# Kernel optimization log

Hardware: AMD Instinct MI355X
Metric: run time of the kernel (lower is better)

The kernel has to match this reference:

```python
import jax, jax.numpy as jnp
import numpy as np
import math

Z, H, G, S = 4, 16, 4, 4096          # batch, q heads, kv groups, seq len
BLOCK = 32                            # compression block size
NB = S // BLOCK                       # number of compressed KV blocks (128)
DQK, DV = 128, 128                    # head dims


def setup_inputs() -> dict:
    key = jax.random.key(0)
    k1, k2, k3 = jax.random.split(key, 3)
    q = jax.random.normal(k1, (Z, H, S, DQK), jnp.float32)
    k_blocks = jax.random.normal(k2, (Z, G, NB, DQK), jnp.float32)
    v_blocks = jax.random.normal(k3, (Z, G, NB, DV), jnp.float32)
    # block j covers tokens [j*BLOCK, (j+1)*BLOCK), so it 'ends' at position (j+1)*BLOCK-1
    block_ends = (jnp.arange(1, NB + 1) * BLOCK - 1).astype(jnp.int32)
    return {"q": q, "k_blocks": k_blocks, "v_blocks": v_blocks, "block_ends": block_ends}


def reference(q, k_blocks, v_blocks, block_ends):
    """NSA compression attention fwd: block-end causal masking over compressed KV blocks.
    q: [Z,H,S,Dqk]; k_blocks/v_blocks: [Z,G,NB,D]; block_ends: [NB] int.
    Query at position m attends to compressed block j iff block_ends[j] <= m.
    Rows with no valid block output zeros (matching the kernel's l_i==0 path)."""
    Zb, Hb, Sb, Dq = q.shape
    Gb = k_blocks.shape[1]
    sm_scale = 1.0 / math.sqrt(Dq)
    # GQA: head h -> kv group h // (H // G)
    qg = (q * sm_scale).reshape(Zb, Gb, Hb // Gb, Sb, Dq)
    s = jnp.einsum('zghsd,zgnd->zghsn', qg, k_blocks)        # [Z,G,H/G,S,NB]
    pos = jnp.arange(Sb)
    mask = block_ends[None, :] <= pos[:, None]               # [S,NB]
    s_masked = jnp.where(mask, s, -jnp.inf)
    m = jnp.max(s_masked, axis=-1, keepdims=True)            # online-softmax max (M)
    m_safe = jnp.where(jnp.isfinite(m), m, 0.0)
    p = jnp.where(mask, jnp.exp(s_masked - jax.lax.stop_gradient(m_safe)), 0.0)
    l = jnp.sum(p, axis=-1, keepdims=True)                   # softmax denom (exp(L-M))
    o = jnp.einsum('zghsn,zgnv->zghsv', p, v_blocks)
    o = jnp.where(l > 0, o / jnp.where(l > 0, l, 1.0), 0.0)
    return o.reshape(Zb, Hb, Sb, -1)                         # [Z,H,S,Dv]
```

## Files before the change

### kernel.cpp

```cpp
#include <hip/hip_runtime.h>


#define Zc 4
#define Hc 16
#define Gc 4
#define Sc 4096
#define NBc 128
#define Dc 128
#define VST 136

typedef __attribute__((ext_vector_type(8))) short short8;
typedef __attribute__((ext_vector_type(4))) float float4v;

__device__ inline unsigned pk2bf(float a, float b) {
    union { float f; unsigned u; } x, y; x.f = a; y.f = b;
    return __builtin_amdgcn_perm(y.u + 0x8000u, x.u + 0x8000u, 0x07060302u);
}
__device__ inline short8 mkfrag(float4v f0, float4v f1) {
    union { short8 v; unsigned d[4]; } u;
    u.d[0] = pk2bf(f0[0], f0[1]);
    u.d[1] = pk2bf(f0[2], f0[3]);
    u.d[2] = pk2bf(f1[0], f1[1]);
    u.d[3] = pk2bf(f1[2], f1[3]);
    return u.v;
}

__global__ __launch_bounds__(256, 4)
void nsa_fwd(const float* __restrict__ q, const float* __restrict__ kb,
             const float* __restrict__ vb, float* __restrict__ out) {
    __shared__ __align__(16) short KV[NBc * VST];

    const int bx   = blockIdx.x, m0 = bx * 128;
    const int h    = blockIdx.y, z = blockIdx.z, g = h >> 2;
    const int tid  = threadIdx.x;
    const int wq   = tid >> 6;
    const int lane = tid & 63;
    const int l16  = lane & 15;
    const int quad = lane >> 4;

    const int nvmax   = 4 * bx + 4;
    const int c_max   = (nvmax + 15) >> 4;
    const int kbi_max = (nvmax + 31) >> 5;
    const int nstage  = kbi_max << 5;

    const float* qbase = q + ((size_t)(z * Hc + h) * Sc + m0 + wq * 32) * Dc;
    float4v qraw[4][2][2];
    #pragma unroll
    for (int dk = 0; dk < 4; dk++)
        #pragma unroll
        for (int t = 0; t < 2; t++) {
            const float* s = qbase + (size_t)(t * 16 + l16) * Dc + dk * 32 + quad * 8;
            qraw[dk][t][0] = *(const float4v*)s;
            qraw[dk][t][1] = *(const float4v*)(s + 4);
        }

    const float* ksrc = kb + (size_t)(z * Gc + g) * NBc * Dc;
    #pragma unroll
    for (int it = 0; it < 8; it++)
        if (it < c_max) {
            int i = it * 256 + tid;
            int n = i >> 4, c8 = i & 15;
            const float* s = ksrc + (size_t)n * Dc + c8 * 8;
            float4v f0 = *(const float4v*)s, f1 = *(const float4v*)(s + 4);
            *(short8*)(KV + n * VST + c8 * 8) = mkfrag(f0, f1);
        }

    const float sm = 0.08838834764831845f;
    short8 qf[4][2];
    #pragma unroll
    for (int dk = 0; dk < 4; dk++)
        #pragma unroll
        for (int t = 0; t < 2; t++)
            qf[dk][t] = mkfrag(qraw[dk][t][0] * sm, qraw[dk][t][1] * sm);

    __syncthreads();

    float4v acc[8][2];
    #pragma unroll
    for (int c = 0; c < 8; c++)
        #pragma unroll
        for (int t = 0; t < 2; t++) acc[c][t] = (float4v)0.f;

    #pragma unroll
    for (int dk = 0; dk < 4; dk++)
        #pragma unroll
        for (int c = 0; c < 8; c++)
            if (c < c_max) {
                short8 a = *(const short8*)(KV + (c * 16 + l16) * VST + dk * 32 + quad * 8);
                acc[c][0] = __builtin_amdgcn_mfma_f32_16x16x32_bf16(a, qf[dk][0], acc[c][0], 0, 0, 0);
                acc[c][1] = __builtin_amdgcn_mfma_f32_16x16x32_bf16(a, qf[dk][1], acc[c][1], 0, 0, 0);
            }

    __syncthreads();

    {
        const float* vsrc = vb + (size_t)(z * Gc + g) * NBc * Dc;
        const int np = tid & 63, n2 = np * 2;
        const bool vact = (n2 < nstage);
        #pragma unroll
        for (int it = 0; it < 8; it++) {
            const int c = it * 4 + wq;
            if (vact) {
                float4v fa = *(const float4v*)(vsrc + (size_t)n2 * Dc + c * 4);
                float4v fb = *(const float4v*)(vsrc + (size_t)(n2 + 1) * Dc + c * 4);
                #pragma unroll
                for (int k2 = 0; k2 < 4; k2++)
                    *(unsigned*)(KV + (c * 4 + k2) * VST + n2) = pk2bf(fa[k2], fb[k2]);
            }
        }
    }

    unsigned Ppk[8][2][2];
    #pragma unroll
    for (int c = 0; c < 8; c++)
        #pragma unroll
        for (int t = 0; t < 2; t++) { Ppk[c][t][0] = 0u; Ppk[c][t][1] = 0u; }

    #pragma unroll
    for (int t = 0; t < 2; t++) {
        const int mg = m0 + wq * 32 + t * 16 + l16;
        int nv = (mg + 1) >> 5; if (nv > NBc) nv = NBc;
        float mx = -1e30f;
        #pragma unroll
        for (int c = 0; c < 8; c++)
            if (c < c_max)
                #pragma unroll
                for (int r = 0; r < 4; r++) {
                    const int j = c * 16 + quad * 4 + r;
                    float s = acc[c][t][r];
                    s = (j < nv) ? s : -1e30f;
                    acc[c][t][r] = s;
                    mx = fmaxf(mx, s);
                }
        mx = fmaxf(mx, __shfl_xor(mx, 16, 64));
        mx = fmaxf(mx, __shfl_xor(mx, 32, 64));
        float ls = 0.f;
        #pragma unroll
        for (int c = 0; c < 8; c++)
            if (c < c_max)
                #pragma unroll
                for (int r = 0; r < 4; r++) {
                    float s = acc[c][t][r];
                    float p = (s > -1e29f) ? __expf(s - mx) : 0.f;
                    acc[c][t][r] = p;
                    ls += p;
                }
        ls += __shfl_xor(ls, 16, 64);
        ls += __shfl_xor(ls, 32, 64);
        const float inv = (ls > 0.f) ? 1.f / ls : 0.f;
        #pragma unroll
        for (int c = 0; c < 8; c++)
            if (c < c_max) {
                Ppk[c][t][0] = pk2bf(acc[c][t][0] * inv, acc[c][t][1] * inv);
                Ppk[c][t][1] = pk2bf(acc[c][t][2] * inv, acc[c][t][3] * inv);
            }
    }

    __syncthreads();

    float4v oacc[8][2];
    #pragma unroll
    for (int c = 0; c < 8; c++)
        #pragma unroll
        for (int t = 0; t < 2; t++) oacc[c][t] = (float4v)0.f;

    const int s0 = (((2 * quad) & 3) << 4) | l16;
    const int s1 = (((2 * quad + 1) & 3) << 4) | l16;
    const bool hi = (quad >= 2);

    #pragma unroll
    for (int kbi = 0; kbi < 4; kbi++)
        if (kbi < kbi_max) {
            short8 ap[2];
            #pragma unroll
            for (int t = 0; t < 2; t++) {
                const int c1 = 2 * kbi;
                unsigned w0a = (unsigned)__shfl((int)Ppk[c1    ][t][0], s0, 64);
                unsigned w0b = (unsigned)__shfl((int)Ppk[c1 + 1][t][0], s0, 64);
                unsigned w1a = (unsigned)__shfl((int)Ppk[c1    ][t][1], s0, 64);
                unsigned w1b = (unsigned)__shfl((int)Ppk[c1 + 1][t][1], s0, 64);
                unsigned w2a = (unsigned)__shfl((int)Ppk[c1    ][t][0], s1, 64);
                unsigned w2b = (unsigned)__shfl((int)Ppk[c1 + 1][t][0], s1, 64);
                unsigned w3a = (unsigned)__shfl((int)Ppk[c1    ][t][1], s1, 64);
                unsigned w3b = (unsigned)__shfl((int)Ppk[c1 + 1][t][1], s1, 64);
                union { short8 v; unsigned d[4]; } u;
                u.d[0] = hi ? w0b : w0a;
                u.d[1] = hi ? w1b : w1a;
                u.d[2] = hi ? w2b : w2a;
                u.d[3] = hi ? w3b : w3a;
                ap[t] = u.v;
            }
            #pragma unroll
            for (int c = 0; c < 8; c++) {
                short8 bv = *(const short8*)(KV + (c * 16 + l16) * VST + kbi * 32 + quad * 8);
                #pragma unroll
                for (int t = 0; t < 2; t++)
                    oacc[c][t] = __builtin_amdgcn_mfma_f32_16x16x32_bf16(ap[t], bv, oacc[c][t], 0, 0, 0);
            }
        }

    float* obase = out + ((size_t)(z * Hc + h) * Sc + m0 + wq * 32) * Dc;
    #pragma unroll
    for (int t = 0; t < 2; t++)
        #pragma unroll
        for (int rr = 0; rr < 4; rr++) {
            const int row = t * 16 + quad * 4 + rr;
            #pragma unroll
            for (int c = 0; c < 8; c++)
                obase[(size_t)row * Dc + c * 16 + l16] = oacc[c][t][rr];
        }
}

extern "C" void kernel_launch(void* const* d_in, const int* in_sizes, int n_in,
                              void* d_out, int out_size, void* d_ws, size_t ws_size,
                              hipStream_t stream) {
    const float* q  = (const float*)d_in[0];
    const float* kb = (const float*)d_in[1];
    const float* vb = (const float*)d_in[2];
    float* out = (float*)d_out;
    dim3 grid(Sc / 128, Hc, Zc);
    nsa_fwd<<<grid, dim3(256), 0, stream>>>(q, kb, vb, out);
}
```

Before: 257.4 us.

## Pair causal query tiles per block to balance work and share KV staging

Each block now handles two 128-row query tiles, b and 31-b, so every block does roughly the same amount of causal work. The K and V blocks are staged to LDS once for both tiles. Per-warp limits (cmax/kbi) now bound the MFMA loops at warp rather than block granularity. The V global loads are issued into registers ahead of the second QK GEMM to overlap latency, which raises register pressure; the launch bound drops to 2 blocks per CU and the grid halves to 1024 blocks.

```diff
diff --git a/kernel.cpp b/kernel.cpp
--- a/kernel.cpp
+++ b/kernel.cpp
@@ -25,100 +25,32 @@
     return u.v;
 }
 
-__global__ __launch_bounds__(256, 4)
-void nsa_fwd(const float* __restrict__ q, const float* __restrict__ kb,
-             const float* __restrict__ vb, float* __restrict__ out) {
-    __shared__ __align__(16) short KV[NBc * VST];
-
-    const int bx   = blockIdx.x, m0 = bx * 128;
-    const int h    = blockIdx.y, z = blockIdx.z, g = h >> 2;
-    const int tid  = threadIdx.x;
-    const int wq   = tid >> 6;
-    const int lane = tid & 63;
-    const int l16  = lane & 15;
-    const int quad = lane >> 4;
-
-    const int nvmax   = 4 * bx + 4;
-    const int c_max   = (nvmax + 15) >> 4;
-    const int kbi_max = (nvmax + 31) >> 5;
-    const int nstage  = kbi_max << 5;
-
-    const float* qbase = q + ((size_t)(z * Hc + h) * Sc + m0 + wq * 32) * Dc;
-    float4v qraw[4][2][2];
-    #pragma unroll
-    for (int dk = 0; dk < 4; dk++)
-        #pragma unroll
-        for (int t = 0; t < 2; t++) {
-            const float* s = qbase + (size_t)(t * 16 + l16) * Dc + dk * 32 + quad * 8;
-            qraw[dk][t][0] = *(const float4v*)s;
-            qraw[dk][t][1] = *(const float4v*)(s + 4);
-        }
-
-    const float* ksrc = kb + (size_t)(z * Gc + g) * NBc * Dc;
-    #pragma unroll
-    for (int it = 0; it < 8; it++)
-        if (it < c_max) {
-            int i = it * 256 + tid;
-            int n = i >> 4, c8 = i & 15;
-            const float* s = ksrc + (size_t)n * Dc + c8 * 8;
-            float4v f0 = *(const float4v*)s, f1 = *(const float4v*)(s + 4);
-            *(short8*)(KV + n * VST + c8 * 8) = mkfrag(f0, f1);
-        }
-
-    const float sm = 0.08838834764831845f;
-    short8 qf[4][2];
-    #pragma unroll
-    for (int dk = 0; dk < 4; dk++)
-        #pragma unroll
-        for (int t = 0; t < 2; t++)
-            qf[dk][t] = mkfrag(qraw[dk][t][0] * sm, qraw[dk][t][1] * sm);
-
-    __syncthreads();
-
-    float4v acc[8][2];
+__device__ inline void do_gemm1(const short* __restrict__ Ksh, short8 (&qf)[4][2],
+                                float4v (&acc)[8][2], int c_max, int l16, int quad) {
     #pragma unroll
     for (int c = 0; c < 8; c++)
         #pragma unroll
         for (int t = 0; t < 2; t++) acc[c][t] = (float4v)0.f;
-
     #pragma unroll
     for (int dk = 0; dk < 4; dk++)
         #pragma unroll
         for (int c = 0; c < 8; c++)
             if (c < c_max) {
-                short8 a = *(const short8*)(KV + (c * 16 + l16) * VST + dk * 32 + quad * 8);
+                short8 a = *(const short8*)(Ksh + (c * 16 + l16) * VST + dk * 32 + quad * 8);
                 acc[c][0] = __builtin_amdgcn_mfma_f32_16x16x32_bf16(a, qf[dk][0], acc[c][0], 0, 0, 0);
                 acc[c][1] = __builtin_amdgcn_mfma_f32_16x16x32_bf16(a, qf[dk][1], acc[c][1], 0, 0, 0);
             }
-
-    __syncthreads();
-
-    {
-        const float* vsrc = vb + (size_t)(z * Gc + g) * NBc * Dc;
-        const int np = tid & 63, n2 = np * 2;
-        const bool vact = (n2 < nstage);
-        #pragma unroll
-        for (int it = 0; it < 8; it++) {
-            const int c = it * 4 + wq;
-            if (vact) {
-                float4v fa = *(const float4v*)(vsrc + (size_t)n2 * Dc + c * 4);
-                float4v fb = *(const float4v*)(vsrc + (size_t)(n2 + 1) * Dc + c * 4);
-                #pragma unroll
-                for (int k2 = 0; k2 < 4; k2++)
-                    *(unsigned*)(KV + (c * 4 + k2) * VST + n2) = pk2bf(fa[k2], fb[k2]);
-            }
-        }
-    }
-
-    unsigned Ppk[8][2][2];
+}
+
+__device__ inline void do_softmax(float4v (&acc)[8][2], unsigned (&Ppk)[8][2][2],
+                                  int m0, int c_max, int l16, int quad) {
     #pragma unroll
     for (int c = 0; c < 8; c++)
         #pragma unroll
         for (int t = 0; t < 2; t++) { Ppk[c][t][0] = 0u; Ppk[c][t][1] = 0u; }
-
     #pragma unroll
     for (int t = 0; t < 2; t++) {
-        const int mg = m0 + wq * 32 + t * 16 + l16;
+        const int mg = m0 + t * 16 + l16;
         int nv = (mg + 1) >> 5; if (nv > NBc) nv = NBc;
         float mx = -1e30f;
         #pragma unroll
@@ -155,9 +87,11 @@
                 Ppk[c][t][1] = pk2bf(acc[c][t][2] * inv, acc[c][t][3] * inv);
             }
     }
-
-    __syncthreads();
-
+}
+
+__device__ inline void do_gemm2_store(const short* __restrict__ Vt, unsigned (&Ppk)[8][2][2],
+                                      float* __restrict__ obase, int kbi_max,
+                                      int l16, int quad) {
     float4v oacc[8][2];
     #pragma unroll
     for (int c = 0; c < 8; c++)
@@ -192,14 +126,13 @@
             }
             #pragma unroll
             for (int c = 0; c < 8; c++) {
-                short8 bv = *(const short8*)(KV + (c * 16 + l16) * VST + kbi * 32 + quad * 8);
+                short8 bv = *(const short8*)(Vt + (c * 16 + l16) * VST + kbi * 32 + quad * 8);
                 #pragma unroll
                 for (int t = 0; t < 2; t++)
                     oacc[c][t] = __builtin_amdgcn_mfma_f32_16x16x32_bf16(ap[t], bv, oacc[c][t], 0, 0, 0);
             }
         }
 
-    float* obase = out + ((size_t)(z * Hc + h) * Sc + m0 + wq * 32) * Dc;
     #pragma unroll
     for (int t = 0; t < 2; t++)
         #pragma unroll
@@ -209,6 +142,122 @@
             for (int c = 0; c < 8; c++)
                 obase[(size_t)row * Dc + c * 16 + l16] = oacc[c][t][rr];
         }
+}
+
+__global__ __launch_bounds__(256, 2)
+void nsa_fwd(const float* __restrict__ q, const float* __restrict__ kb,
+             const float* __restrict__ vb, float* __restrict__ out) {
+    __shared__ __align__(16) short KV[NBc * VST];
+
+    const int b    = blockIdx.x;
+    const int h    = blockIdx.y, z = blockIdx.z, g = h >> 2;
+    const int tid  = threadIdx.x;
+    const int wq   = tid >> 6;
+    const int lane = tid & 63;
+    const int l16  = lane & 15;
+    const int quad = lane >> 4;
+
+    const int bx0 = b, bx1 = 31 - b;
+    const int nv0 = 4 * bx0 + wq + 1;
+    const int nv1 = 4 * bx1 + wq + 1;
+    const int cmax0 = (nv0 + 15) >> 4, kbi0 = (nv0 + 31) >> 5;
+    const int cmax1 = (nv1 + 15) >> 4, kbi1 = (nv1 + 31) >> 5;
+    const int nv_hi  = 4 * bx1 + 4;
+    const int cst    = (nv_hi + 15) >> 4;
+    const int nstage = ((nv_hi + 31) >> 5) << 5;
+
+    const int m0_0 = bx0 * 128 + wq * 32;
+    const int m0_1 = bx1 * 128 + wq * 32;
+    const float sm = 0.08838834764831845f;
+
+    const float* qb0 = q + ((size_t)(z * Hc + h) * Sc + m0_0) * Dc;
+    float4v q0raw[4][2][2];
+    #pragma unroll
+    for (int dk = 0; dk < 4; dk++)
+        #pragma unroll
+        for (int t = 0; t < 2; t++) {
+            const float* s = qb0 + (size_t)(t * 16 + l16) * Dc + dk * 32 + quad * 8;
+            q0raw[dk][t][0] = *(const float4v*)s;
+            q0raw[dk][t][1] = *(const float4v*)(s + 4);
+        }
+
+    const float* ksrc = kb + (size_t)(z * Gc + g) * NBc * Dc;
+    #pragma unroll
+    for (int it = 0; it < 8; it++)
+        if (it < cst) {
+            int i = it * 256 + tid;
+            int n = i >> 4, c8 = i & 15;
+            const float* s = ksrc + (size_t)n * Dc + c8 * 8;
+            float4v f0 = *(const float4v*)s, f1 = *(const float4v*)(s + 4);
+            *(short8*)(KV + n * VST + c8 * 8) = mkfrag(f0, f1);
+        }
+
+    short8 qf[4][2];
+    #pragma unroll
+    for (int dk = 0; dk < 4; dk++)
+        #pragma unroll
+        for (int t = 0; t < 2; t++)
+            qf[dk][t] = mkfrag(q0raw[dk][t][0] * sm, q0raw[dk][t][1] * sm);
+
+    __syncthreads();
+
+    const float* qb1 = q + ((size_t)(z * Hc + h) * Sc + m0_1) * Dc;
+    float4v q1raw[4][2][2];
+    #pragma unroll
+    for (int dk = 0; dk < 4; dk++)
+        #pragma unroll
+        for (int t = 0; t < 2; t++) {
+            const float* s = qb1 + (size_t)(t * 16 + l16) * Dc + dk * 32 + quad * 8;
+            q1raw[dk][t][0] = *(const float4v*)s;
+            q1raw[dk][t][1] = *(const float4v*)(s + 4);
+        }
+
+    float4v acc[8][2];
+    unsigned Ppk0[8][2][2], Ppk1[8][2][2];
+
+    do_gemm1(KV, qf, acc, cmax0, l16, quad);
+    do_softmax(acc, Ppk0, m0_0, cmax0, l16, quad);
+
+    #pragma unroll
+    for (int dk = 0; dk < 4; dk++)
+        #pragma unroll
+        for (int t = 0; t < 2; t++)
+            qf[dk][t] = mkfrag(q1raw[dk][t][0] * sm, q1raw[dk][t][1] * sm);
+
+    const float* vsrc = vb + (size_t)(z * Gc + g) * NBc * Dc;
+    const int n2 = lane * 2;
+    const bool vact = (n2 < nstage);
+    float4v vraw[8][2];
+    #pragma unroll
+    for (int it = 0; it < 8; it++) {
+        const int c = it * 4 + wq;
+        if (vact) {
+            vraw[it][0] = *(const float4v*)(vsrc + (size_t)n2 * Dc + c * 4);
+            vraw[it][1] = *(const float4v*)(vsrc + (size_t)(n2 + 1) * Dc + c * 4);
+        }
+    }
+
+    do_gemm1(KV, qf, acc, cmax1, l16, quad);
+
+    __syncthreads();
+
+    #pragma unroll
+    for (int it = 0; it < 8; it++) {
+        const int c = it * 4 + wq;
+        if (vact) {
+            #pragma unroll
+            for (int k2 = 0; k2 < 4; k2++)
+                *(unsigned*)(KV + (c * 4 + k2) * VST + n2) = pk2bf(vraw[it][0][k2], vraw[it][1][k2]);
+        }
+    }
+    do_softmax(acc, Ppk1, m0_1, cmax1, l16, quad);
+
+    __syncthreads();
+
+    float* ob0 = out + ((size_t)(z * Hc + h) * Sc + m0_0) * Dc;
+    float* ob1 = out + ((size_t)(z * Hc + h) * Sc + m0_1) * Dc;
+    do_gemm2_store(KV, Ppk0, ob0, kbi0, l16, quad);
+    do_gemm2_store(KV, Ppk1, ob1, kbi1, l16, quad);
 }
 
 extern "C" void kernel_launch(void* const* d_in, const int* in_sizes, int n_in,
@@ -218,6 +267,6 @@
     const float* kb = (const float*)d_in[1];
     const float* vb = (const float*)d_in[2];
     float* out = (float*)d_out;
-    dim3 grid(Sc / 128, Hc, Zc);
+    dim3 grid(16, Hc, Zc);
     nsa_fwd<<<grid, dim3(256), 0, stream>>>(q, kb, vb, out);
 }
```

Result: faster. 249.2 us (-3.2%).
